# Kernel optimization log

Hardware: AMD Instinct MI355X
Metric: run time of the kernel (lower is better)

The kernel has to match this reference:

```python
import jax, jax.numpy as jnp
import numpy as np
from jax.scipy.linalg import expm


def setup_inputs() -> dict:
    key = jax.random.key(0)
    k1, k2, k3 = jax.random.split(key, 3)
    B, T, d = 64, 4096, 16
    Z = jax.random.normal(k1, (B, T, 2), dtype=jnp.float32)
    A1 = jax.random.normal(k2, (d, d), dtype=jnp.float32)
    A2 = jax.random.normal(k3, (d, d), dtype=jnp.float32)
    return {"Z": Z, "A1": A1, "A2": A2}


def reference(Z, A1, A2):
    # Z: [B, T, 2]; A1, A2: [d, d] learned params
    d = A1.shape[0]
    S1 = A1 - A1.T  # skew-symmetric
    S2 = A2 - A2.T
    # per-timestep increment matrices: expm(z1*S1 + z2*S2), shape [B, T, d, d]
    G = Z[..., 0, None, None] * S1 + Z[..., 1, None, None] * S2
    M = expm(G)
    # X_0 = I; X_t = X_{t-1} @ M[:, t] for t = 1..T-1  (M[:, 0] is unused,
    # exactly as in the original loop starting at t=1).
    matmul = lambda a, b: jnp.einsum('...ij,...jk->...ik', a, b)
    prefix = jax.lax.associative_scan(matmul, M[:, 1:], axis=1)  # [B, T-1, d, d]
    eye = jnp.broadcast_to(jnp.eye(d, dtype=Z.dtype), (Z.shape[0], 1, d, d))
    A = jnp.concatenate([eye, prefix], axis=1)  # [B, T, d, d]
    B_inv = jnp.linalg.inv(A)
    return (A, B_inv)
```

## Files before the change

### kernel.cpp

```cpp
#include <hip/hip_runtime.h>

#define NB 64
#define NT 4096
#define CH 16
#define KC (NT/CH)
#define GPB 16
#define ROWB 72
#define MATS (4*ROWB)
#define LGS (2*MATS + 8)
#define BX 0
#define BY MATS
#define NA 128
#define PI_F 3.14159265358979f

#define WSYNC() asm volatile("s_waitcnt lgkmcnt(0)" ::: "memory")

#define MM_FMA(A_, B0_, B1_, B2_, B3_, base) \
  acc[base+0] = fmaf(A_.w, B3_.x, fmaf(A_.z, B2_.x, fmaf(A_.y, B1_.x, fmaf(A_.x, B0_.x, acc[base+0])))); \
  acc[base+1] = fmaf(A_.w, B3_.y, fmaf(A_.z, B2_.y, fmaf(A_.y, B1_.y, fmaf(A_.x, B0_.y, acc[base+1])))); \
  acc[base+2] = fmaf(A_.w, B3_.z, fmaf(A_.z, B2_.z, fmaf(A_.y, B1_.z, fmaf(A_.x, B0_.z, acc[base+2])))); \
  acc[base+3] = fmaf(A_.w, B3_.w, fmaf(A_.z, B2_.w, fmaf(A_.y, B1_.w, fmaf(A_.x, B0_.w, acc[base+3]))));

template<bool CLR>
__device__ __forceinline__ void mmg(float acc[16], const float* sb, int offA, int offB,
                                    const int xA[4], const int xB[4], int trR) {
  if (CLR) {
#pragma unroll
    for (int e = 0; e < 16; ++e) acc[e] = 0.f;
  }
#pragma unroll
  for (int kk = 0; kk < 4; ++kk) {
    const float* pa = sb + offA + trR + xA[kk];
    const float* pb = sb + offB + kk*ROWB + xB[kk];
    float4 a0 = *(const float4*)(pa +  0);
    float4 a1 = *(const float4*)(pa + 16);
    float4 a2 = *(const float4*)(pa + 32);
    float4 a3 = *(const float4*)(pa + 48);
    float4 b0 = *(const float4*)(pb +  0);
    float4 b1 = *(const float4*)(pb + 16);
    float4 b2 = *(const float4*)(pb + 32);
    float4 b3 = *(const float4*)(pb + 48);
    MM_FMA(a0, b0, b1, b2, b3, 0)
    MM_FMA(a1, b0, b1, b2, b3, 4)
    MM_FMA(a2, b0, b1, b2, b3, 8)
    MM_FMA(a3, b0, b1, b2, b3, 12)
  }
}

__device__ __forceinline__ void st4(float* sb, int offD, const float v[16], int trR, int xD) {
  float* p = sb + offD + trR + xD;
#pragma unroll
  for (int rr = 0; rr < 4; ++rr)
    *(float4*)(p + rr*16) = make_float4(v[rr*4+0], v[rr*4+1], v[rr*4+2], v[rr*4+3]);
}

__global__ __launch_bounds__(128) void k0_spec(const float* __restrict__ A1,
                                               const float* __restrict__ A2,
                                               float* __restrict__ ws) {
  __shared__ float S1[256], S2[256];
  const int tid = threadIdx.x;
  for (int e = tid; e < 256; e += 128) {
    int i_ = e >> 4, j_ = e & 15;
    S1[e] = A1[i_*16+j_] - A1[j_*16+i_];
    S2[e] = A2[i_*16+j_] - A2[j_*16+i_];
  }
  __syncthreads();
  const float th = (float)tid * (PI_F / NA);
  const float c = cosf(th), s = sinf(th);
  float v[16];
  float n2 = 0.f;
#pragma unroll
  for (int j = 0; j < 16; ++j) { v[j] = sinf(1.7f*(float)(j+1) + th) + 0.25f; n2 += v[j]*v[j]; }
  float inv = rsqrtf(n2);
#pragma unroll
  for (int j = 0; j < 16; ++j) v[j] *= inv;
  float lam = 0.f;
  for (int it = 0; it < 14; ++it) {
    float w[16];
#pragma unroll
    for (int i = 0; i < 16; ++i) {
      float a1 = 0.f, a2 = 0.f;
#pragma unroll
      for (int j = 0; j < 16; ++j) { a1 = fmaf(S1[i*16+j], v[j], a1); a2 = fmaf(S2[i*16+j], v[j], a2); }
      w[i] = c*a1 + s*a2;
    }
    n2 = 0.f;
#pragma unroll
    for (int i = 0; i < 16; ++i) n2 += w[i]*w[i];
    lam = sqrtf(n2);
    inv = (lam > 1e-20f) ? 1.f/lam : 0.f;
#pragma unroll
    for (int i = 0; i < 16; ++i) v[i] = w[i]*inv;
  }
  ws[tid] = lam * 1.05f;
}

__global__ __launch_bounds__(256, 2) void k1_chunk(const float* __restrict__ Z,
                                                   const float* __restrict__ A1,
                                                   const float* __restrict__ A2,
                                                   const float* __restrict__ ws,
                                                   float* __restrict__ Aout)
{
  __shared__ __align__(16) float lds[GPB * LGS];
  __shared__ float rhos[NA];
  const int tid = threadIdx.x;
  const int g   = tid >> 4;
  const int u   = tid & 15;
  const int tr  = u >> 2;
  const int tc  = u & 3;
  const int gw  = (tid & 63) >> 4;
  const int trR = tr * ROWB;

  if (tid < NA) rhos[tid] = ws[tid];
  __syncthreads();

  float* sb = lds + g * LGS;
  const int xA[4] = { ((0^tr)<<2), ((1^tr)<<2), ((2^tr)<<2), ((3^tr)<<2) };
  const int xB[4] = { ((tc^0)<<2), ((tc^1)<<2), ((tc^2)<<2), ((tc^3)<<2) };
  const int xD    = ((tc^tr)<<2);

  const int cid    = blockIdx.x * GPB + g;
  const int b      = cid >> 8;
  const int kchunk = cid & (KC-1);
  const int t0     = kchunk * CH;

  const float trtc = (tr == tc) ? 1.f : 0.f;
  float s1t[16], s2t[16];
#pragma unroll
  for (int rr = 0; rr < 4; ++rr)
#pragma unroll
    for (int cc = 0; cc < 4; ++cc) {
      int r_ = 4*tr + rr, c_ = 4*tc + cc;
      s1t[rr*4+cc] = A1[r_*16 + c_] - A1[c_*16 + r_];
      s2t[rr*4+cc] = A2[r_*16 + c_] - A2[c_*16 + r_];
    }

  float2 za = *(const float2*)&Z[(size_t)(b*NT + t0 + u) * 2];

  float lt[16], acc[16], gt[16], pp[16], uu[16];
#pragma unroll
  for (int rr = 0; rr < 4; ++rr)
#pragma unroll
    for (int cc = 0; cc < 4; ++cc) lt[rr*4+cc] = (rr == cc) ? trtc : 0.f;

  const float C3 = 1.f/6.f,   C4 = 1.f/24.f,   C5 = 1.f/120.f,
              C6 = 1.f/720.f, C7 = 1.f/5040.f, C8 = 1.f/40320.f;

  for (int tt = 0; tt < CH; ++tt) {
    const int t = t0 + tt;
    const size_t obase = (size_t)(b*NT + t) * 256 + (size_t)(tr*64) + 4*tc;

    const int src = (gw << 4) + tt;
    float z1 = __shfl(za.x, src);
    float z2 = __shfl(za.y, src);
    float r_  = sqrtf(z1*z1 + z2*z2);
    float th  = atan2f(z2, z1);
    if (th < 0.f) th += PI_F;
    int   idx = ((int)(th * ((float)NA / PI_F) + 0.5f)) & (NA - 1);
    float nrm = r_ * rhos[idx];
    nrm = fmaxf(nrm, __shfl_xor(nrm, 16));
    nrm = fmaxf(nrm, __shfl_xor(nrm, 32));
    int s = 0;
    if (nrm > 1.0f) s = (int)ceilf(log2f(nrm));
    const float scl = exp2f(-(float)s);

    if (kchunk == 0 && tt == 0) {
#pragma unroll
      for (int rr = 0; rr < 4; ++rr)
        *(float4*)&Aout[obase + rr*16] =
          make_float4(lt[rr*4+0], lt[rr*4+1], lt[rr*4+2], lt[rr*4+3]);
      continue;
    }
    z1 *= scl; z2 *= scl;

#pragma unroll
    for (int e = 0; e < 16; ++e) gt[e] = z1*s1t[e] + z2*s2t[e];
    st4(sb, BX, gt, trR, xD);  WSYNC();

    mmg<true>(acc, sb, BX, BX, xA, xB, trR);
    st4(sb, BY, acc, trR, xD);
#pragma unroll
    for (int e = 0; e < 16; ++e) {
      pp[e] = gt[e] + 0.5f*acc[e];
      uu[e] = C5*gt[e] + C6*acc[e];
    }
    pp[0] += trtc; pp[5] += trtc; pp[10] += trtc; pp[15] += trtc;
    uu[0] += C4*trtc; uu[5] += C4*trtc; uu[10] += C4*trtc; uu[15] += C4*trtc;
    WSYNC();

    mmg<true>(acc, sb, BY, BX, xA, xB, trR);
#pragma unroll
    for (int e = 0; e < 16; ++e) { pp[e] += C3*acc[e]; uu[e] += C7*acc[e]; }
    mmg<true>(acc, sb, BY, BY, xA, xB, trR);
#pragma unroll
    for (int e = 0; e < 16; ++e) uu[e] += C8*acc[e];
    st4(sb, BX, acc, trR, xD);
    st4(sb, BY, uu, trR, xD);
    WSYNC();

    mmg<false>(pp, sb, BX, BY, xA, xB, trR);
    int cur = BY, oth = BX;
    st4(sb, cur, pp, trR, xD); WSYNC();

    for (int q = 0; q < s; ++q) {
      mmg<true>(acc, sb, cur, cur, xA, xB, trR);
      st4(sb, oth, acc, trR, xD); WSYNC();
      int tmp = cur; cur = oth; oth = tmp;
    }

    st4(sb, oth, lt, trR, xD); WSYNC();
    mmg<true>(acc, sb, oth, cur, xA, xB, trR);
#pragma unroll
    for (int e = 0; e < 16; ++e) lt[e] = acc[e];

#pragma unroll
    for (int rr = 0; rr < 4; ++rr)
      *(float4*)&Aout[obase + rr*16] =
        make_float4(lt[rr*4+0], lt[rr*4+1], lt[rr*4+2], lt[rr*4+3]);
  }
}

__global__ __launch_bounds__(256) void k2a(const float* __restrict__ Aout,
                                           float* __restrict__ Binv) {
  __shared__ float Cy[256], Lt[256];
  const int tid = threadIdx.x, i = tid >> 4, j = tid & 15;
  const int b = blockIdx.x >> 4, sb = blockIdx.x & 15;
  Cy[tid] = (i == j) ? 1.f : 0.f;
  float nxt = Aout[((size_t)(b*NT + (sb*16)*CH + CH - 1))*256 + tid];
  __syncthreads();
  for (int q = 0; q < 16; ++q) {
    const int k = sb*16 + q;
    Binv[((size_t)(b*NT + k*CH))*256 + tid] = Cy[tid];
    Lt[tid] = nxt;
    __syncthreads();
    if (q < 15) nxt = Aout[((size_t)(b*NT + (k+1)*CH + CH - 1))*256 + tid];
    float a2 = 0.f;
#pragma unroll
    for (int m = 0; m < 16; ++m) a2 = fmaf(Cy[i*16+m], Lt[m*16+j], a2);
    __syncthreads();
    Cy[tid] = a2;
    __syncthreads();
  }
  Binv[((size_t)(b*NT + sb*256 + 1))*256 + tid] = Cy[tid];
}

__global__ __launch_bounds__(256) void k2b(float* __restrict__ Binv) {
  __shared__ float Cy[256], Lt[256];
  const int tid = threadIdx.x, i = tid >> 4, j = tid & 15;
  const int b = blockIdx.x;
  Cy[tid] = (i == j) ? 1.f : 0.f;
  float nxt = Binv[((size_t)(b*NT + 1))*256 + tid];
  __syncthreads();
  for (int sb2 = 0; sb2 < 16; ++sb2) {
    Binv[((size_t)(b*NT + sb2*256 + 2))*256 + tid] = Cy[tid];
    Lt[tid] = nxt;
    __syncthreads();
    if (sb2 < 15) nxt = Binv[((size_t)(b*NT + (sb2+1)*256 + 1))*256 + tid];
    float a2 = 0.f;
#pragma unroll
    for (int m = 0; m < 16; ++m) a2 = fmaf(Cy[i*16+m], Lt[m*16+j], a2);
    __syncthreads();
    Cy[tid] = a2;
    __syncthreads();
  }
}

__global__ __launch_bounds__(256, 2) void k3_apply(float* __restrict__ Aout,
                                                   float* __restrict__ Binv)
{
  __shared__ __align__(16) float lds[GPB * LGS];
  __shared__ float SupL[256];
  const int tid = threadIdx.x;
  const int g   = tid >> 4;
  const int u   = tid & 15;
  const int tr  = u >> 2;
  const int tc  = u & 3;
  const int trR = tr * ROWB;
  float* sb_ = lds + g * LGS;
  const int xA[4] = { ((0^tr)<<2), ((1^tr)<<2), ((2^tr)<<2), ((3^tr)<<2) };
  const int xB[4] = { ((tc^0)<<2), ((tc^1)<<2), ((tc^2)<<2), ((tc^3)<<2) };
  const int xD    = ((tc^tr)<<2);

  const int b   = blockIdx.x >> 4;
  const int sbq = blockIdx.x & 15;
  const int k   = sbq*16 + g;
  const int t0  = k * CH;

  SupL[tid] = Binv[((size_t)(b*NT + sbq*256 + 2))*256 + tid];
  {
    const float* srcp = &Binv[((size_t)(b*NT + k*CH))*256];
#pragma unroll
    for (int rr = 0; rr < 4; ++rr) {
      float4 v = *(const float4*)&srcp[rr*64 + 4*u];
      *(float4*)&sb_[BX + rr*ROWB + tr*16 + ((tc^rr)<<2)] = v;
    }
  }
  __syncthreads();

  float wt[16];
  {
    float* acc = wt;
#pragma unroll
    for (int e = 0; e < 16; ++e) acc[e] = 0.f;
#pragma unroll
    for (int kk = 0; kk < 4; ++kk) {
      const float* pb = sb_ + BX + kk*ROWB + xB[kk];
      float4 b0 = *(const float4*)(pb +  0);
      float4 b1 = *(const float4*)(pb + 16);
      float4 b2 = *(const float4*)(pb + 32);
      float4 b3 = *(const float4*)(pb + 48);
      float4 a0 = *(const float4*)&SupL[(4*tr+0)*16 + 4*kk];
      float4 a1 = *(const float4*)&SupL[(4*tr+1)*16 + 4*kk];
      float4 a2 = *(const float4*)&SupL[(4*tr+2)*16 + 4*kk];
      float4 a3 = *(const float4*)&SupL[(4*tr+3)*16 + 4*kk];
      MM_FMA(a0, b0, b1, b2, b3, 0)
      MM_FMA(a1, b0, b1, b2, b3, 4)
      MM_FMA(a2, b0, b1, b2, b3, 8)
      MM_FMA(a3, b0, b1, b2, b3, 12)
    }
  }
  st4(sb_, BY, wt, trR, xD);
  WSYNC();

  float acc[16];
  for (int tt = 0; tt < CH; ++tt) {
    const size_t base = ((size_t)(b*NT + t0 + tt))*256;
#pragma unroll
    for (int rr = 0; rr < 4; ++rr) {
      float4 v = *(const float4*)&Aout[base + rr*64 + 4*u];
      *(float4*)&sb_[BX + rr*ROWB + tr*16 + ((tc^rr)<<2)] = v;
    }
    WSYNC();
    mmg<true>(acc, sb_, BY, BX, xA, xB, trR);
    const size_t obase = base + (size_t)(tr*64) + 4*tc;
#pragma unroll
    for (int rr = 0; rr < 4; ++rr)
      *(float4*)&Aout[obase + rr*16] =
        make_float4(acc[rr*4+0], acc[rr*4+1], acc[rr*4+2], acc[rr*4+3]);
    st4(sb_, BX, acc, trR, xD); WSYNC();
    const float* pt = sb_ + BX + tc*ROWB + ((tr^tc)<<2);
    float4 f0 = *(const float4*)(pt +  0);
    float4 f1 = *(const float4*)(pt + 16);
    float4 f2 = *(const float4*)(pt + 32);
    float4 f3 = *(const float4*)(pt + 48);
    *(float4*)&Binv[obase +  0] = make_float4(f0.x, f1.x, f2.x, f3.x);
    *(float4*)&Binv[obase + 16] = make_float4(f0.y, f1.y, f2.y, f3.y);
    *(float4*)&Binv[obase + 32] = make_float4(f0.z, f1.z, f2.z, f3.z);
    *(float4*)&Binv[obase + 48] = make_float4(f0.w, f1.w, f2.w, f3.w);
    WSYNC();
  }
}

extern "C" void kernel_launch(void* const* d_in, const int* in_sizes, int n_in,
                              void* d_out, int out_size, void* d_ws, size_t ws_size,
                              hipStream_t stream) {
  const float* Z  = (const float*)d_in[0];
  const float* A1 = (const float*)d_in[1];
  const float* A2 = (const float*)d_in[2];
  float* ws   = (float*)d_ws;
  float* Aout = (float*)d_out;
  float* Binv = Aout + (size_t)NB * NT * 256;

  k0_spec<<<1, 128, 0, stream>>>(A1, A2, ws);
  k1_chunk<<<NB * KC / GPB, 256, 0, stream>>>(Z, A1, A2, ws, Aout);
  k2a<<<NB * 16, 256, 0, stream>>>(Aout, Binv);
  k2b<<<64, 256, 0, stream>>>(Binv);
  k3_apply<<<NB * 16, 256, 0, stream>>>(Aout, Binv);
}
```

Measured before the change: 614.7 us.

## Precompute monomial expansion of generator powers and use register DPP matmuls

A prep kernel now precomputes the symmetrized products of S1 and S2 up to degree four once, so each timestep builds G, G^2, G^3 and G^4 as scalar polynomial combinations of 14 cached matrices in LDS. This replaces three 16x16 matmuls per step. The remaining matmuls (the Horner-style combine, the squaring loop and the prefix update) now exchange data across lanes in registers with DPP and ds_swizzle instead of staging through LDS. In exchange, every step reads 14 matrices from LDS and the kernel uses more registers, which may lower occupancy.

```diff
diff --git a/kernel.cpp b/kernel.cpp
--- a/kernel.cpp
+++ b/kernel.cpp
@@ -5,14 +5,251 @@
 #define CH 16
 #define KC (NT/CH)
 #define GPB 16
+#define NA 128
+#define NM 14
+#define PI_F 3.14159265358979f
+
+#define C3c (1.f/6.f)
+#define C4c (1.f/24.f)
+#define C5c (1.f/120.f)
+#define C6c (1.f/720.f)
+#define C7c (1.f/5040.f)
+#define C8c (1.f/40320.f)
+
+template<int K>
+__device__ __forceinline__ void mm_step(float acc[16], const float a[16], const float b[16]) {
+  float bb[16];
+#pragma unroll
+  for (int e = 0; e < 16; ++e)
+    bb[e] = __int_as_float(__builtin_amdgcn_ds_swizzle(__float_as_int(b[e]), (K << 7) | 0x13));
+#pragma unroll
+  for (int rr = 0; rr < 4; ++rr) {
+    const float a0 = __int_as_float(__builtin_amdgcn_mov_dpp(__float_as_int(a[rr*4+0]), K*0x55, 0xF, 0xF, true));
+    const float a1 = __int_as_float(__builtin_amdgcn_mov_dpp(__float_as_int(a[rr*4+1]), K*0x55, 0xF, 0xF, true));
+    const float a2 = __int_as_float(__builtin_amdgcn_mov_dpp(__float_as_int(a[rr*4+2]), K*0x55, 0xF, 0xF, true));
+    const float a3 = __int_as_float(__builtin_amdgcn_mov_dpp(__float_as_int(a[rr*4+3]), K*0x55, 0xF, 0xF, true));
+#pragma unroll
+    for (int cc = 0; cc < 4; ++cc)
+      acc[rr*4+cc] = fmaf(a3, bb[12+cc], fmaf(a2, bb[8+cc], fmaf(a1, bb[4+cc], fmaf(a0, bb[cc], acc[rr*4+cc]))));
+  }
+}
+__device__ __forceinline__ void mmreg(float acc[16], const float a[16], const float b[16]) {
+  mm_step<0>(acc, a, b); mm_step<1>(acc, a, b);
+  mm_step<2>(acc, a, b); mm_step<3>(acc, a, b);
+}
+
+__global__ __launch_bounds__(256) void k0_prep(const float* __restrict__ A1,
+                                               const float* __restrict__ A2,
+                                               float* __restrict__ ws) {
+  __shared__ float S[2][256], W2[4][256], W3[8][256], W4[16][256];
+  const int tid = threadIdx.x;
+  {
+    int i_ = tid >> 4, j_ = tid & 15;
+    S[0][tid] = A1[i_*16+j_] - A1[j_*16+i_];
+    S[1][tid] = A2[i_*16+j_] - A2[j_*16+i_];
+  }
+  __syncthreads();
+  const int i = tid >> 4, j = tid & 15;
+#pragma unroll
+  for (int p = 0; p < 4; ++p) {
+    const float* a = S[p>>1]; const float* bm = S[p&1];
+    float acc = 0.f;
+    for (int k = 0; k < 16; ++k) acc = fmaf(a[i*16+k], bm[k*16+j], acc);
+    W2[p][tid] = acc;
+  }
+  __syncthreads();
+#pragma unroll
+  for (int p = 0; p < 8; ++p) {
+    const float* a = S[p>>2]; const float* bm = W2[p&3];
+    float acc = 0.f;
+    for (int k = 0; k < 16; ++k) acc = fmaf(a[i*16+k], bm[k*16+j], acc);
+    W3[p][tid] = acc;
+  }
+  __syncthreads();
+#pragma unroll
+  for (int p = 0; p < 16; ++p) {
+    const float* a = S[p>>3]; const float* bm = W3[p&7];
+    float acc = 0.f;
+    for (int k = 0; k < 16; ++k) acc = fmaf(a[i*16+k], bm[k*16+j], acc);
+    W4[p][tid] = acc;
+  }
+  __syncthreads();
+  float* M = ws + NA;
+  M[ 0*256+tid] = S[0][tid];
+  M[ 1*256+tid] = S[1][tid];
+  M[ 2*256+tid] = W2[0][tid];
+  M[ 3*256+tid] = W2[1][tid] + W2[2][tid];
+  M[ 4*256+tid] = W2[3][tid];
+  M[ 5*256+tid] = W3[0][tid];
+  M[ 6*256+tid] = W3[1][tid] + W3[2][tid] + W3[4][tid];
+  M[ 7*256+tid] = W3[3][tid] + W3[5][tid] + W3[6][tid];
+  M[ 8*256+tid] = W3[7][tid];
+  M[ 9*256+tid] = W4[0][tid];
+  M[10*256+tid] = W4[1][tid] + W4[2][tid] + W4[4][tid] + W4[8][tid];
+  M[11*256+tid] = W4[3][tid] + W4[5][tid] + W4[6][tid] + W4[9][tid] + W4[10][tid] + W4[12][tid];
+  M[12*256+tid] = W4[7][tid] + W4[11][tid] + W4[13][tid] + W4[14][tid];
+  M[13*256+tid] = W4[15][tid];
+  if (tid < NA) {
+    const float th = (float)tid * (PI_F / NA);
+    const float c = cosf(th), s = sinf(th);
+    float v[16];
+    float n2 = 0.f;
+#pragma unroll
+    for (int jj = 0; jj < 16; ++jj) { v[jj] = sinf(1.7f*(float)(jj+1) + th) + 0.25f; n2 += v[jj]*v[jj]; }
+    float inv = rsqrtf(n2);
+#pragma unroll
+    for (int jj = 0; jj < 16; ++jj) v[jj] *= inv;
+    float lam = 0.f;
+    for (int it = 0; it < 14; ++it) {
+      float w[16];
+#pragma unroll
+      for (int ii = 0; ii < 16; ++ii) {
+        float a1 = 0.f, a2 = 0.f;
+#pragma unroll
+        for (int jj = 0; jj < 16; ++jj) { a1 = fmaf(S[0][ii*16+jj], v[jj], a1); a2 = fmaf(S[1][ii*16+jj], v[jj], a2); }
+        w[ii] = c*a1 + s*a2;
+      }
+      n2 = 0.f;
+#pragma unroll
+      for (int ii = 0; ii < 16; ++ii) n2 += w[ii]*w[ii];
+      lam = sqrtf(n2);
+      inv = (lam > 1e-20f) ? 1.f/lam : 0.f;
+#pragma unroll
+      for (int ii = 0; ii < 16; ++ii) v[ii] = w[ii]*inv;
+    }
+    ws[tid] = lam * 1.05f;
+  }
+}
+
+__global__ __launch_bounds__(256, 2) void k1_chunk(const float* __restrict__ Z,
+                                                   const float* __restrict__ wsrc,
+                                                   float* __restrict__ Aout)
+{
+  __shared__ float Qs[NM*256];
+  __shared__ float rhos[NA];
+  const int tid = threadIdx.x;
+  for (int e = tid; e < NM*256; e += 256) Qs[e] = wsrc[NA + e];
+  if (tid < NA) rhos[tid] = wsrc[tid];
+  __syncthreads();
+
+  const int g  = tid >> 4;
+  const int u  = tid & 15;
+  const int tr = u >> 2;
+  const int tc = u & 3;
+  const int gw = (tid & 63) >> 4;
+  const int qbase = (4*tr)*16 + 4*tc;
+
+  const int cid    = blockIdx.x * GPB + g;
+  const int b      = cid >> 8;
+  const int kchunk = cid & (KC-1);
+  const int t0     = kchunk * CH;
+
+  const float trtc = (tr == tc) ? 1.f : 0.f;
+  float2 za = *(const float2*)&Z[(size_t)(b*NT + t0 + u) * 2];
+
+  float lt[16];
+#pragma unroll
+  for (int rr = 0; rr < 4; ++rr)
+#pragma unroll
+    for (int cc = 0; cc < 4; ++cc) lt[rr*4+cc] = (rr == cc) ? trtc : 0.f;
+
+  for (int tt = 0; tt < CH; ++tt) {
+    const size_t obase = (size_t)(b*NT + t0 + tt) * 256 + (size_t)(tr*64) + 4*tc;
+
+    const int src = (gw << 4) + tt;
+    float z1 = __shfl(za.x, src);
+    float z2 = __shfl(za.y, src);
+    float r_ = sqrtf(z1*z1 + z2*z2);
+    float th = atan2f(z2, z1);
+    if (th < 0.f) th += PI_F;
+    int idx = ((int)(th * ((float)NA / PI_F) + 0.5f)) & (NA - 1);
+    float nrm = r_ * rhos[idx];
+    nrm = fmaxf(nrm, __shfl_xor(nrm, 16));
+    nrm = fmaxf(nrm, __shfl_xor(nrm, 32));
+    int s = 0;
+    if (nrm > 1.0f) s = (int)ceilf(log2f(nrm));
+    const float scl = exp2f(-(float)s);
+
+    if (kchunk == 0 && tt == 0) {
+#pragma unroll
+      for (int rr = 0; rr < 4; ++rr)
+        *(float4*)&Aout[obase + rr*16] =
+          make_float4(lt[rr*4+0], lt[rr*4+1], lt[rr*4+2], lt[rr*4+3]);
+      continue;
+    }
+
+    const float x = z1*scl, y = z2*scl;
+    const float x2 = x*x, xy = x*y, y2 = y*y;
+    const float x3 = x2*x, x2y = x2*y, xy2 = x*y2, y3 = y2*y;
+    const float zc[NM] = { x, y, x2, xy, y2, x3, x2y, xy2, y3,
+                           x2*x2, x3*y, x2*y2, x*y3, y2*y2 };
+    const float WP[NM] = { 1.f,1.f, .5f,.5f,.5f, C3c,C3c,C3c,C3c, 0.f,0.f,0.f,0.f,0.f };
+    const float WU[NM] = { C5c,C5c, C6c,C6c,C6c, C7c,C7c,C7c,C7c, C8c,C8c,C8c,C8c,C8c };
+
+    float pp[16], uu[16], g4[16];
+#pragma unroll
+    for (int rr = 0; rr < 4; ++rr)
+#pragma unroll
+      for (int cc = 0; cc < 4; ++cc) {
+        pp[rr*4+cc] = (rr == cc) ? trtc : 0.f;
+        uu[rr*4+cc] = (rr == cc) ? trtc * C4c : 0.f;
+        g4[rr*4+cc] = 0.f;
+      }
+#pragma unroll
+    for (int m = 0; m < NM; ++m) {
+      const float am = zc[m] * WP[m];
+      const float bm = zc[m] * WU[m];
+#pragma unroll
+      for (int rr = 0; rr < 4; ++rr) {
+        float4 v = *(const float4*)&Qs[m*256 + rr*16 + qbase];
+        if (m < 9) {
+          pp[rr*4+0] = fmaf(am, v.x, pp[rr*4+0]);
+          pp[rr*4+1] = fmaf(am, v.y, pp[rr*4+1]);
+          pp[rr*4+2] = fmaf(am, v.z, pp[rr*4+2]);
+          pp[rr*4+3] = fmaf(am, v.w, pp[rr*4+3]);
+        } else {
+          g4[rr*4+0] = fmaf(zc[m], v.x, g4[rr*4+0]);
+          g4[rr*4+1] = fmaf(zc[m], v.y, g4[rr*4+1]);
+          g4[rr*4+2] = fmaf(zc[m], v.z, g4[rr*4+2]);
+          g4[rr*4+3] = fmaf(zc[m], v.w, g4[rr*4+3]);
+        }
+        uu[rr*4+0] = fmaf(bm, v.x, uu[rr*4+0]);
+        uu[rr*4+1] = fmaf(bm, v.y, uu[rr*4+1]);
+        uu[rr*4+2] = fmaf(bm, v.z, uu[rr*4+2]);
+        uu[rr*4+3] = fmaf(bm, v.w, uu[rr*4+3]);
+      }
+    }
+
+    mmreg(pp, g4, uu);
+
+    for (int q = 0; q < s; ++q) {
+      float acc[16];
+#pragma unroll
+      for (int e = 0; e < 16; ++e) acc[e] = 0.f;
+      mmreg(acc, pp, pp);
+#pragma unroll
+      for (int e = 0; e < 16; ++e) pp[e] = acc[e];
+    }
+    {
+      float acc[16];
+#pragma unroll
+      for (int e = 0; e < 16; ++e) acc[e] = 0.f;
+      mmreg(acc, lt, pp);
+#pragma unroll
+      for (int e = 0; e < 16; ++e) lt[e] = acc[e];
+    }
+#pragma unroll
+    for (int rr = 0; rr < 4; ++rr)
+      *(float4*)&Aout[obase + rr*16] =
+        make_float4(lt[rr*4+0], lt[rr*4+1], lt[rr*4+2], lt[rr*4+3]);
+  }
+}
+
 #define ROWB 72
 #define MATS (4*ROWB)
 #define LGS (2*MATS + 8)
 #define BX 0
 #define BY MATS
-#define NA 128
-#define PI_F 3.14159265358979f
-
 #define WSYNC() asm volatile("s_waitcnt lgkmcnt(0)" ::: "memory")
 
 #define MM_FMA(A_, B0_, B1_, B2_, B3_, base) \
@@ -54,172 +291,6 @@
     *(float4*)(p + rr*16) = make_float4(v[rr*4+0], v[rr*4+1], v[rr*4+2], v[rr*4+3]);
 }
 
-__global__ __launch_bounds__(128) void k0_spec(const float* __restrict__ A1,
-                                               const float* __restrict__ A2,
-                                               float* __restrict__ ws) {
-  __shared__ float S1[256], S2[256];
-  const int tid = threadIdx.x;
-  for (int e = tid; e < 256; e += 128) {
-    int i_ = e >> 4, j_ = e & 15;
-    S1[e] = A1[i_*16+j_] - A1[j_*16+i_];
-    S2[e] = A2[i_*16+j_] - A2[j_*16+i_];
-  }
-  __syncthreads();
-  const float th = (float)tid * (PI_F / NA);
-  const float c = cosf(th), s = sinf(th);
-  float v[16];
-  float n2 = 0.f;
-#pragma unroll
-  for (int j = 0; j < 16; ++j) { v[j] = sinf(1.7f*(float)(j+1) + th) + 0.25f; n2 += v[j]*v[j]; }
-  float inv = rsqrtf(n2);
-#pragma unroll
-  for (int j = 0; j < 16; ++j) v[j] *= inv;
-  float lam = 0.f;
-  for (int it = 0; it < 14; ++it) {
-    float w[16];
-#pragma unroll
-    for (int i = 0; i < 16; ++i) {
-      float a1 = 0.f, a2 = 0.f;
-#pragma unroll
-      for (int j = 0; j < 16; ++j) { a1 = fmaf(S1[i*16+j], v[j], a1); a2 = fmaf(S2[i*16+j], v[j], a2); }
-      w[i] = c*a1 + s*a2;
-    }
-    n2 = 0.f;
-#pragma unroll
-    for (int i = 0; i < 16; ++i) n2 += w[i]*w[i];
-    lam = sqrtf(n2);
-    inv = (lam > 1e-20f) ? 1.f/lam : 0.f;
-#pragma unroll
-    for (int i = 0; i < 16; ++i) v[i] = w[i]*inv;
-  }
-  ws[tid] = lam * 1.05f;
-}
-
-__global__ __launch_bounds__(256, 2) void k1_chunk(const float* __restrict__ Z,
-                                                   const float* __restrict__ A1,
-                                                   const float* __restrict__ A2,
-                                                   const float* __restrict__ ws,
-                                                   float* __restrict__ Aout)
-{
-  __shared__ __align__(16) float lds[GPB * LGS];
-  __shared__ float rhos[NA];
-  const int tid = threadIdx.x;
-  const int g   = tid >> 4;
-  const int u   = tid & 15;
-  const int tr  = u >> 2;
-  const int tc  = u & 3;
-  const int gw  = (tid & 63) >> 4;
-  const int trR = tr * ROWB;
-
-  if (tid < NA) rhos[tid] = ws[tid];
-  __syncthreads();
-
-  float* sb = lds + g * LGS;
-  const int xA[4] = { ((0^tr)<<2), ((1^tr)<<2), ((2^tr)<<2), ((3^tr)<<2) };
-  const int xB[4] = { ((tc^0)<<2), ((tc^1)<<2), ((tc^2)<<2), ((tc^3)<<2) };
-  const int xD    = ((tc^tr)<<2);
-
-  const int cid    = blockIdx.x * GPB + g;
-  const int b      = cid >> 8;
-  const int kchunk = cid & (KC-1);
-  const int t0     = kchunk * CH;
-
-  const float trtc = (tr == tc) ? 1.f : 0.f;
-  float s1t[16], s2t[16];
-#pragma unroll
-  for (int rr = 0; rr < 4; ++rr)
-#pragma unroll
-    for (int cc = 0; cc < 4; ++cc) {
-      int r_ = 4*tr + rr, c_ = 4*tc + cc;
-      s1t[rr*4+cc] = A1[r_*16 + c_] - A1[c_*16 + r_];
-      s2t[rr*4+cc] = A2[r_*16 + c_] - A2[c_*16 + r_];
-    }
-
-  float2 za = *(const float2*)&Z[(size_t)(b*NT + t0 + u) * 2];
-
-  float lt[16], acc[16], gt[16], pp[16], uu[16];
-#pragma unroll
-  for (int rr = 0; rr < 4; ++rr)
-#pragma unroll
-    for (int cc = 0; cc < 4; ++cc) lt[rr*4+cc] = (rr == cc) ? trtc : 0.f;
-
-  const float C3 = 1.f/6.f,   C4 = 1.f/24.f,   C5 = 1.f/120.f,
-              C6 = 1.f/720.f, C7 = 1.f/5040.f, C8 = 1.f/40320.f;
-
-  for (int tt = 0; tt < CH; ++tt) {
-    const int t = t0 + tt;
-    const size_t obase = (size_t)(b*NT + t) * 256 + (size_t)(tr*64) + 4*tc;
-
-    const int src = (gw << 4) + tt;
-    float z1 = __shfl(za.x, src);
-    float z2 = __shfl(za.y, src);
-    float r_  = sqrtf(z1*z1 + z2*z2);
-    float th  = atan2f(z2, z1);
-    if (th < 0.f) th += PI_F;
-    int   idx = ((int)(th * ((float)NA / PI_F) + 0.5f)) & (NA - 1);
-    float nrm = r_ * rhos[idx];
-    nrm = fmaxf(nrm, __shfl_xor(nrm, 16));
-    nrm = fmaxf(nrm, __shfl_xor(nrm, 32));
-    int s = 0;
-    if (nrm > 1.0f) s = (int)ceilf(log2f(nrm));
-    const float scl = exp2f(-(float)s);
-
-    if (kchunk == 0 && tt == 0) {
-#pragma unroll
-      for (int rr = 0; rr < 4; ++rr)
-        *(float4*)&Aout[obase + rr*16] =
-          make_float4(lt[rr*4+0], lt[rr*4+1], lt[rr*4+2], lt[rr*4+3]);
-      continue;
-    }
-    z1 *= scl; z2 *= scl;
-
-#pragma unroll
-    for (int e = 0; e < 16; ++e) gt[e] = z1*s1t[e] + z2*s2t[e];
-    st4(sb, BX, gt, trR, xD);  WSYNC();
-
-    mmg<true>(acc, sb, BX, BX, xA, xB, trR);
-    st4(sb, BY, acc, trR, xD);
-#pragma unroll
-    for (int e = 0; e < 16; ++e) {
-      pp[e] = gt[e] + 0.5f*acc[e];
-      uu[e] = C5*gt[e] + C6*acc[e];
-    }
-    pp[0] += trtc; pp[5] += trtc; pp[10] += trtc; pp[15] += trtc;
-    uu[0] += C4*trtc; uu[5] += C4*trtc; uu[10] += C4*trtc; uu[15] += C4*trtc;
-    WSYNC();
-
-    mmg<true>(acc, sb, BY, BX, xA, xB, trR);
-#pragma unroll
-    for (int e = 0; e < 16; ++e) { pp[e] += C3*acc[e]; uu[e] += C7*acc[e]; }
-    mmg<true>(acc, sb, BY, BY, xA, xB, trR);
-#pragma unroll
-    for (int e = 0; e < 16; ++e) uu[e] += C8*acc[e];
-    st4(sb, BX, acc, trR, xD);
-    st4(sb, BY, uu, trR, xD);
-    WSYNC();
-
-    mmg<false>(pp, sb, BX, BY, xA, xB, trR);
-    int cur = BY, oth = BX;
-    st4(sb, cur, pp, trR, xD); WSYNC();
-
-    for (int q = 0; q < s; ++q) {
-      mmg<true>(acc, sb, cur, cur, xA, xB, trR);
-      st4(sb, oth, acc, trR, xD); WSYNC();
-      int tmp = cur; cur = oth; oth = tmp;
-    }
-
-    st4(sb, oth, lt, trR, xD); WSYNC();
-    mmg<true>(acc, sb, oth, cur, xA, xB, trR);
-#pragma unroll
-    for (int e = 0; e < 16; ++e) lt[e] = acc[e];
-
-#pragma unroll
-    for (int rr = 0; rr < 4; ++rr)
-      *(float4*)&Aout[obase + rr*16] =
-        make_float4(lt[rr*4+0], lt[rr*4+1], lt[rr*4+2], lt[rr*4+3]);
-  }
-}
-
 __global__ __launch_bounds__(256) void k2a(const float* __restrict__ Aout,
                                            float* __restrict__ Binv) {
   __shared__ float Cy[256], Lt[256];
@@ -361,9 +432,9 @@
   float* Aout = (float*)d_out;
   float* Binv = Aout + (size_t)NB * NT * 256;
 
-  k0_spec<<<1, 128, 0, stream>>>(A1, A2, ws);
-  k1_chunk<<<NB * KC / GPB, 256, 0, stream>>>(Z, A1, A2, ws, Aout);
+  k0_prep<<<1, 256, 0, stream>>>(A1, A2, ws);
+  k1_chunk<<<NB * KC / GPB, 256, 0, stream>>>(Z, ws, Aout);
   k2a<<<NB * 16, 256, 0, stream>>>(Aout, Binv);
-  k2b<<<64, 256, 0, stream>>>(Binv);
+  k2b<<<NB, 256, 0, stream>>>(Binv);
   k3_apply<<<NB * 16, 256, 0, stream>>>(Aout, Binv);
 }
```

Result: faster. 538.8 us (-12.3%).
